# Optimization experiments

Measured on AMD Instinct MI355X. Metric: run time of the kernel, lower is better.

Reference implementation:

```python
import jax, jax.numpy as jnp
import numpy as np

B, N, D = 16384, 64, 64

def setup_inputs() -> dict:
    key = jax.random.key(0)
    ks = jax.random.split(key, 8)
    return {
        "self_vectors": jax.random.normal(ks[0], (B, 1, D), dtype=jnp.float32),
        "neighbor_vectors": jax.random.normal(ks[1], (B, 1, N, D), dtype=jnp.float32),
        "neighbor_relations": jax.random.normal(ks[2], (B, 1, N, D), dtype=jnp.float32),
        "user_embeddings": jax.random.normal(ks[3], (B, D), dtype=jnp.float32),
        "W1": jax.random.normal(ks[4], (2 * D, D), dtype=jnp.float32) * (1.0 / np.sqrt(2 * D)),
        "b1": jnp.zeros((D,), dtype=jnp.float32),
        "w2": jax.random.normal(ks[5], (D, 1), dtype=jnp.float32) * (1.0 / np.sqrt(D)),
        "b2": jnp.zeros((1,), dtype=jnp.float32),
    }

def reference(self_vectors, neighbor_vectors, neighbor_relations, user_embeddings, W1, b1, w2, b2):
    b, _, n, d = neighbor_relations.shape
    # user embedding broadcast over neighbors: [b,1,n,d]
    ue = jnp.broadcast_to(user_embeddings[:, None, None, :], (b, 1, n, d))
    head_rel = jnp.concatenate([ue, neighbor_relations], axis=-1)  # [b,1,n,2d]
    hidden = jax.nn.relu(head_rel @ W1 + b1)                        # [b,1,n,d]
    decay = jax.nn.sigmoid(hidden @ w2 + b2)                        # [b,1,n,1]
    decay = jax.nn.softmax(decay, axis=2)                           # softmax over neighbors
    agg = jnp.sum(decay * neighbor_vectors, axis=2)                 # [b,1,d]
    return jnp.concatenate([self_vectors, agg], axis=-1)           # [b,1,2d]
```

## Files before the change

kernel.cpp:

```cpp
#include <hip/hip_runtime.h>
#include <math.h>

#define BATCH 16384
#define NN 64
#define DD 64
#define REL_STRIDE 68

__global__ __launch_bounds__(64)
void aggregator_kernel(const float* __restrict__ self_v,
                       const float* __restrict__ nv,
                       const float* __restrict__ rel,
                       const float* __restrict__ ue,
                       const float* __restrict__ W1,
                       const float* __restrict__ b1,
                       const float* __restrict__ w2,
                       const float* __restrict__ b2,
                       float* __restrict__ out)
{
    const int b = blockIdx.x;
    const int t = threadIdx.x;

    __shared__ float rel_s[NN * REL_STRIDE];
    __shared__ float ue_s[DD];
    __shared__ float u1_s[DD];
    __shared__ float w2_s[DD];
    __shared__ float wbuf[NN];

    const float* relb = rel + (size_t)b * (NN * DD);

    #pragma unroll
    for (int i = 0; i < 16; ++i) {
        int f = i * 256 + t * 4;
        float4 v = *(const float4*)(relb + f);
        int n = f >> 6;
        int k = f & 63;
        *(float4*)(&rel_s[n * REL_STRIDE + k]) = v;
    }
    ue_s[t] = ue[(size_t)b * DD + t];
    w2_s[t] = w2[t];
    __syncthreads();

    {
        float acc = b1[t];
        #pragma unroll 8
        for (int k = 0; k < DD; ++k) {
            acc = fmaf(ue_s[k], W1[k * DD + t], acc);
        }
        u1_s[t] = acc;
    }
    __syncthreads();

    float h[DD];
    #pragma unroll
    for (int j = 0; j < DD; ++j) h[j] = u1_s[j];

    const float* __restrict__ W1b = W1 + DD * DD;
    for (int k = 0; k < DD; ++k) {
        float x = rel_s[t * REL_STRIDE + k];
        const float* __restrict__ row = W1b + k * DD;
        #pragma unroll
        for (int j = 0; j < DD; ++j) h[j] = fmaf(x, row[j], h[j]);
    }

    float d = b2[0];
    #pragma unroll
    for (int j = 0; j < DD; ++j) d = fmaf(fmaxf(h[j], 0.0f), w2_s[j], d);
    float dec = 1.0f / (1.0f + __expf(-d));

    float m = dec;
    #pragma unroll
    for (int off = 32; off > 0; off >>= 1) m = fmaxf(m, __shfl_xor(m, off, 64));
    float e = __expf(dec - m);
    float s = e;
    #pragma unroll
    for (int off = 32; off > 0; off >>= 1) s += __shfl_xor(s, off, 64);
    wbuf[t] = e / s;
    __syncthreads();

    const float* __restrict__ nvb = nv + (size_t)b * (NN * DD);
    float agg = 0.0f;
    #pragma unroll 8
    for (int n = 0; n < NN; ++n) {
        agg = fmaf(wbuf[n], nvb[n * DD + t], agg);
    }

    out[(size_t)b * (2 * DD) + t]      = self_v[(size_t)b * DD + t];
    out[(size_t)b * (2 * DD) + DD + t] = agg;
}

extern "C" void kernel_launch(void* const* d_in, const int* in_sizes, int n_in,
                              void* d_out, int out_size, void* d_ws, size_t ws_size,
                              hipStream_t stream) {
    const float* self_v = (const float*)d_in[0];
    const float* nv     = (const float*)d_in[1];
    const float* rel    = (const float*)d_in[2];
    const float* ue     = (const float*)d_in[3];
    const float* W1     = (const float*)d_in[4];
    const float* b1     = (const float*)d_in[5];
    const float* w2     = (const float*)d_in[6];
    const float* b2     = (const float*)d_in[7];
    float* out = (float*)d_out;

    aggregator_kernel<<<dim3(BATCH), dim3(64), 0, stream>>>(
        self_v, nv, rel, ue, W1, b1, w2, b2, out);
}
```

Before: 599.6 us.

## Split hidden dimension across four waves per block with shared-memory reductions

The block grows from 64 to 256 threads, and each of the four waves computes 16 of the 64 hidden units for all neighbors. Partial decay logits, user projections and aggregation partials are reduced through shared memory. This cuts per-thread register use (h[64] becomes h[16]) and the serial FMA chain per thread, which should raise occupancy and latency hiding. The rel tile padding changes to stride 65 with scalar stores, and the cost is extra syncthreads and reduction traffic.

```diff
diff --git a/kernel.cpp b/kernel.cpp
--- a/kernel.cpp
+++ b/kernel.cpp
@@ -4,9 +4,9 @@
 #define BATCH 16384
 #define NN 64
 #define DD 64
-#define REL_STRIDE 68
+#define RS 65
 
-__global__ __launch_bounds__(64)
+__global__ __launch_bounds__(256, 8)
 void aggregator_kernel(const float* __restrict__ self_v,
                        const float* __restrict__ nv,
                        const float* __restrict__ rel,
@@ -17,75 +17,97 @@
                        const float* __restrict__ b2,
                        float* __restrict__ out)
 {
-    const int b = blockIdx.x;
-    const int t = threadIdx.x;
+    const int b    = blockIdx.x;
+    const int t    = threadIdx.x;
+    const int lane = t & 63;
+    const int w    = t >> 6;
 
-    __shared__ float rel_s[NN * REL_STRIDE];
-    __shared__ float ue_s[DD];
+    __shared__ float rel_s[NN * RS];
+    __shared__ float red[4 * 64];
     __shared__ float u1_s[DD];
-    __shared__ float w2_s[DD];
     __shared__ float wbuf[NN];
 
-    const float* relb = rel + (size_t)b * (NN * DD);
+    const float*  relb = rel + (size_t)b * (NN * DD);
+    const float4* rel4 = (const float4*)relb;
 
     #pragma unroll
-    for (int i = 0; i < 16; ++i) {
-        int f = i * 256 + t * 4;
-        float4 v = *(const float4*)(relb + f);
-        int n = f >> 6;
-        int k = f & 63;
-        *(float4*)(&rel_s[n * REL_STRIDE + k]) = v;
+    for (int c = 0; c < 4; ++c) {
+        int f = t + 256 * c;
+        float4 v = rel4[f];
+        int n = f >> 4, kq = f & 15;
+        float* dst = &rel_s[n * RS + kq * 4];
+        dst[0] = v.x; dst[1] = v.y; dst[2] = v.z; dst[3] = v.w;
     }
-    ue_s[t] = ue[(size_t)b * DD + t];
-    w2_s[t] = w2[t];
+
+    {
+        const float* ueb = ue + (size_t)b * DD + w * 16;
+        const float* W1a = W1 + (w * 16) * DD + lane;
+        float acc = 0.0f;
+        #pragma unroll
+        for (int k = 0; k < 16; ++k) acc = fmaf(ueb[k], W1a[k * DD], acc);
+        red[t] = acc;
+    }
+    __syncthreads();
+
+    if (t < 64)
+        u1_s[t] = b1[t] + red[t] + red[64 + t] + red[128 + t] + red[192 + t];
+    __syncthreads();
+
+    const int j0 = w * 16;
+    float h[16];
+    #pragma unroll
+    for (int jj = 0; jj < 16; ++jj) h[jj] = u1_s[j0 + jj];
+
+    const float* __restrict__ rrow = &rel_s[lane * RS];
+    const float* __restrict__ W1b  = W1 + DD * DD + j0;
+    #pragma unroll 8
+    for (int k = 0; k < DD; ++k) {
+        float x = rrow[k];
+        const float* __restrict__ row = W1b + k * DD;
+        #pragma unroll
+        for (int jj = 0; jj < 16; ++jj) h[jj] = fmaf(x, row[jj], h[jj]);
+    }
+
+    {
+        const float* w2s = w2 + j0;
+        float p = 0.0f;
+        #pragma unroll
+        for (int jj = 0; jj < 16; ++jj) p = fmaf(fmaxf(h[jj], 0.0f), w2s[jj], p);
+        red[t] = p;
+    }
+    __syncthreads();
+
+    if (t < 64) {
+        float d = b2[0] + red[t] + red[64 + t] + red[128 + t] + red[192 + t];
+        float dec = 1.0f / (1.0f + __expf(-d));
+        float m = dec;
+        #pragma unroll
+        for (int off = 32; off > 0; off >>= 1) m = fmaxf(m, __shfl_xor(m, off, 64));
+        float e = __expf(dec - m);
+        float s = e;
+        #pragma unroll
+        for (int off = 32; off > 0; off >>= 1) s += __shfl_xor(s, off, 64);
+        wbuf[t] = e / s;
+    }
     __syncthreads();
 
     {
-        float acc = b1[t];
-        #pragma unroll 8
-        for (int k = 0; k < DD; ++k) {
-            acc = fmaf(ue_s[k], W1[k * DD + t], acc);
-        }
-        u1_s[t] = acc;
+        const float* nvb = nv + (size_t)b * (NN * DD) + (w * 16) * DD + lane;
+        float ap = 0.0f;
+        #pragma unroll
+        for (int i = 0; i < 16; ++i)
+            ap = fmaf(wbuf[w * 16 + i], nvb[i * DD], ap);
+        red[t] = ap;
     }
     __syncthreads();
 
-    float h[DD];
-    #pragma unroll
-    for (int j = 0; j < DD; ++j) h[j] = u1_s[j];
-
-    const float* __restrict__ W1b = W1 + DD * DD;
-    for (int k = 0; k < DD; ++k) {
-        float x = rel_s[t * REL_STRIDE + k];
-        const float* __restrict__ row = W1b + k * DD;
-        #pragma unroll
-        for (int j = 0; j < DD; ++j) h[j] = fmaf(x, row[j], h[j]);
+    if (t < 64) {
+        out[(size_t)b * (2 * DD) + t] = self_v[(size_t)b * DD + t];
+    } else if (t < 128) {
+        int j = t - 64;
+        out[(size_t)b * (2 * DD) + DD + j] =
+            red[j] + red[64 + j] + red[128 + j] + red[192 + j];
     }
-
-    float d = b2[0];
-    #pragma unroll
-    for (int j = 0; j < DD; ++j) d = fmaf(fmaxf(h[j], 0.0f), w2_s[j], d);
-    float dec = 1.0f / (1.0f + __expf(-d));
-
-    float m = dec;
-    #pragma unroll
-    for (int off = 32; off > 0; off >>= 1) m = fmaxf(m, __shfl_xor(m, off, 64));
-    float e = __expf(dec - m);
-    float s = e;
-    #pragma unroll
-    for (int off = 32; off > 0; off >>= 1) s += __shfl_xor(s, off, 64);
-    wbuf[t] = e / s;
-    __syncthreads();
-
-    const float* __restrict__ nvb = nv + (size_t)b * (NN * DD);
-    float agg = 0.0f;
-    #pragma unroll 8
-    for (int n = 0; n < NN; ++n) {
-        agg = fmaf(wbuf[n], nvb[n * DD + t], agg);
-    }
-
-    out[(size_t)b * (2 * DD) + t]      = self_v[(size_t)b * DD + t];
-    out[(size_t)b * (2 * DD) + DD + t] = agg;
 }
 
 extern "C" void kernel_launch(void* const* d_in, const int* in_sizes, int n_in,
@@ -101,6 +123,6 @@
     const float* b2     = (const float*)d_in[7];
     float* out = (float*)d_out;
 
-    aggregator_kernel<<<dim3(BATCH), dim3(64), 0, stream>>>(
+    aggregator_kernel<<<dim3(BATCH), dim3(256), 0, stream>>>(
         self_v, nv, rel, ue, W1, b1, w2, b2, out);
 }
```

Measured after the change: 928.1 us. 1.55x slower.
